# Performance work log

Measured on AMD Instinct MI355X. Metric: run time of the kernel, lower is better.

Reference implementation:

```python
import jax, jax.numpy as jnp
import numpy as np

T, B, D = 4096, 8, 256  # tgt_len, batch, embed dim
P, O = 256, 256         # proj_dim, out_dim


def setup_inputs() -> dict:
    key = jax.random.key(0)
    k1, k2, k3, k4, k5 = jax.random.split(key, 5)
    return {
        "query": jax.random.normal(k1, (T, B, D), dtype=jnp.float32),
        "W_kqv": jax.random.normal(k2, (D, 3 * P), dtype=jnp.float32) * (D ** -0.5),
        "b_kqv": jax.random.normal(k3, (3 * P,), dtype=jnp.float32) * 0.02,
        "W_out": jax.random.normal(k4, (P, O), dtype=jnp.float32) * (P ** -0.5),
        "b_out": jax.random.normal(k5, (O,), dtype=jnp.float32) * 0.02,
    }


def reference(query, W_kqv, b_kqv, W_out, b_out):
    # query: [T, B, D] (Time x Batch x Channel)
    p = W_kqv.shape[1] // 3
    scaling = p ** -0.5
    qkv = query @ W_kqv + b_kqv                      # [T, B, 3P]
    q, k, v = jnp.split(qkv, 3, axis=-1)             # each [T, B, P]
    q = (q * scaling).transpose(1, 0, 2)             # [B, T, P]
    k = k.transpose(1, 0, 2)                         # [B, S, P] (S == T)
    v = v.transpose(1, 0, 2)                         # [B, S, P]
    scores = jnp.einsum('btp,bsp->bts', q, k)        # [B, T, S]
    probs = jax.nn.softmax(scores.astype(jnp.float32), axis=-1).astype(q.dtype)
    attn = jnp.einsum('bts,bsp->btp', probs, v)      # [B, T, P]
    attn = attn.transpose(1, 0, 2)                   # [T, B, P]
    return attn @ W_out + b_out                      # [T, B, O]
```

## Files before the change

kernel.cpp:

```cpp
#include <hip/hip_runtime.h>
#include <hip/hip_bf16.h>

#define T_LEN 4096
#define BATCH 8
#define D_DIM 256
#define P_DIM 256
#define O_DIM 256
#define N3    768

typedef __bf16 bf16;
typedef __attribute__((ext_vector_type(8))) __bf16 bf16x8;
typedef __attribute__((ext_vector_type(4))) __bf16 bf16x4;
typedef __attribute__((ext_vector_type(4))) float f32x4;
typedef __attribute__((ext_vector_type(16))) float f32x16;

#define MFMA16(a, b, c) __builtin_amdgcn_mfma_f32_16x16x32_bf16(a, b, c, 0, 0, 0)
#define MFMA32(a, b, c) __builtin_amdgcn_mfma_f32_32x32x16_bf16(a, b, c, 0, 0, 0)

#define LDS_P 72

#define BARRIER_LGKM() __asm__ __volatile__("s_waitcnt lgkmcnt(0)\n\ts_barrier" ::: "memory")
#define BARRIER_VM(N) __asm__ __volatile__("s_waitcnt vmcnt(" #N ")\n\ts_barrier" ::: "memory")

typedef __attribute__((address_space(1))) const unsigned int g_u32;
typedef __attribute__((address_space(3))) unsigned int l_u32;
#define GLD16(gp, lp) __builtin_amdgcn_global_load_lds((g_u32*)(gp), (l_u32*)(lp), 16, 0, 0)

__device__ __forceinline__ void wpack_body(
    const float* __restrict__ src, bf16* __restrict__ dst, int ncols, int g)
{
    const int lane = g & 63;
    const int idx = g >> 6;
    const int nt = idx & 3, kt = (idx >> 2) & 7, ch = idx >> 5;
    const int n = ch * 64 + nt * 16 + (lane & 15);
    const int kb = kt * 32 + (lane >> 4) * 8;
    bf16x8 pk;
    #pragma unroll
    for (int j = 0; j < 8; ++j) pk[j] = (bf16)src[(size_t)(kb + j) * ncols + n];
    *(bf16x8*)&dst[(size_t)g * 8] = pk;
}

__global__ __launch_bounds__(256) void wpack_all_kernel(
    const float* __restrict__ W_kqv, const float* __restrict__ W_out,
    bf16* __restrict__ wkp, bf16* __restrict__ wop)
{
    const int bid = blockIdx.x;
    if (bid < 96) {
        wpack_body(W_kqv, wkp, N3, bid * 256 + threadIdx.x);
    } else {
        wpack_body(W_out, wop, O_DIM, (bid - 96) * 256 + threadIdx.x);
    }
}

__global__ __launch_bounds__(256) void qkv_proj_kernel(
    const float* __restrict__ query, const bf16* __restrict__ wkp,
    const float* __restrict__ b_kqv,
    bf16* __restrict__ qb, bf16* __restrict__ kpk, bf16* __restrict__ vpk)
{
    __shared__ __align__(16) bf16 Tt[64][72];
    __shared__ __align__(16) bf16 Wb[2][16384];
    const int m0 = blockIdx.x * 64;
    const int t0g = m0 >> 3;
    const int tid = threadIdx.x;
    const int lane = tid & 63, wave = tid >> 6, l15 = lane & 15, quad = lane >> 4;
    const int arow = wave * 16 + l15;

#define STAGE_W(CH, NB)                                                       \
    {                                                                         \
        const bf16* gsrc = wkp + (size_t)(CH) * 16384;                        \
        _Pragma("unroll")                                                     \
        for (int j = 0; j < 8; ++j)                                           \
            GLD16(gsrc + ((size_t)j * 256 + tid) * 8,                         \
                  &Wb[NB][(j * 256 + wave * 64) * 8]);                        \
    }

    STAGE_W(0, 0);

    bf16x8 af[8];
    {
        const float* qsrc = query + (size_t)(m0 + arow) * D_DIM + quad * 8;
        #pragma unroll
        for (int kt = 0; kt < 8; ++kt) {
            float4 f0 = *(const float4*)(qsrc + kt * 32);
            float4 f1 = *(const float4*)(qsrc + kt * 32 + 4);
            af[kt] = bf16x8{(bf16)f0.x, (bf16)f0.y, (bf16)f0.z, (bf16)f0.w,
                            (bf16)f1.x, (bf16)f1.y, (bf16)f1.z, (bf16)f1.w};
        }
    }

    for (int ch = 0; ch < 12; ++ch) {
        const int buf = ch & 1;
        if (ch < 11) {
            STAGE_W(ch + 1, buf ^ 1);
            BARRIER_VM(8);
        } else {
            BARRIER_VM(0);
        }

        f32x4 acc[4];
        #pragma unroll
        for (int i = 0; i < 4; ++i)
            for (int r = 0; r < 4; ++r) acc[i][r] = 0.f;
        #pragma unroll
        for (int kt = 0; kt < 8; ++kt) {
            #pragma unroll
            for (int nt = 0; nt < 4; ++nt) {
                bf16x8 bb = *(const bf16x8*)&Wb[buf][((kt * 4 + nt) * 64 + lane) * 8];
                acc[nt] = MFMA16(af[kt], bb, acc[nt]);
            }
        }

        BARRIER_LGKM();

        if (ch < 8) {
            const float scale = (ch < 4) ? 0.0625f : 1.0f;
            #pragma unroll
            for (int nt = 0; nt < 4; ++nt) {
                const int c = ch * 64 + nt * 16 + l15;
                const float bias = b_kqv[c];
                #pragma unroll
                for (int r = 0; r < 4; ++r)
                    Tt[wave * 16 + quad * 4 + r][nt * 16 + l15]
                        = (bf16)((acc[nt][r] + bias) * scale);
            }
            BARRIER_LGKM();
            if (ch < 4) {
                #pragma unroll
                for (int uu = 0; uu < 2; ++uu) {
                    const int u = tid * 2 + uu;
                    const int row = u >> 3, cl = u & 7;
                    bf16x8 pk = *(const bf16x8*)&Tt[row][cl * 8];
                    const int m = m0 + row, t = m >> 3, bi = m & 7;
                    *(bf16x8*)&qb[((size_t)bi * T_LEN + t) * P_DIM + ch * 64 + cl * 8] = pk;
                }
            } else {
                #pragma unroll
                for (int uu = 0; uu < 2; ++uu) {
                    const int u = tid * 2 + uu;
                    const int cl = u >> 6, bi = (u >> 3) & 7, idx = u & 7;
                    const int row = idx * 8 + bi;
                    bf16x8 pk = *(const bf16x8*)&Tt[row][cl * 8];
                    const int t = t0g + idx;
                    const int st32 = t >> 5, n31 = t & 31;
                    const int c16 = (ch - 4) * 4 + (cl >> 1), halfk = cl & 1;
                    *(bf16x8*)&kpk[(size_t)((((bi * 128 + st32) * 16 + c16) * 64
                                             + halfk * 32 + n31) * 8)] = pk;
                }
            }
        } else {
            #pragma unroll
            for (int nt = 0; nt < 4; ++nt) {
                const int c = ch * 64 + nt * 16 + l15;
                const float bias = b_kqv[c];
                #pragma unroll
                for (int r = 0; r < 4; ++r)
                    Tt[nt * 16 + l15][wave * 16 + quad * 4 + r] = (bf16)(acc[nt][r] + bias);
            }
            BARRIER_LGKM();
            const int s64 = t0g >> 6, ks = (t0g >> 4) & 3, halfv = (t0g >> 3) & 1;
            #pragma unroll
            for (int uu = 0; uu < 2; ++uu) {
                const int u = tid * 2 + uu;
                const int cl = u >> 3, bi = u & 7;
                bf16x8 pk;
                #pragma unroll
                for (int j = 0; j < 8; ++j) pk[j] = Tt[cl][j * 8 + bi];
                const int cc = (ch - 8) * 64 + cl;
                const int ptG = cc >> 5, n31 = cc & 31;
                *(bf16x8*)&vpk[((((size_t)bi * 64 + s64) * 4 + ks) * 8 + ptG) * 512
                               + (size_t)(halfv * 32 + n31) * 8] = pk;
            }
        }
    }
#undef STAGE_W
}

__global__ __launch_bounds__(256, 2) void flash_attn_kernel(
    const bf16* __restrict__ qb, const bf16* __restrict__ kpk,
    const bf16* __restrict__ vpk, const bf16* __restrict__ wop,
    const float* __restrict__ b_out, float* __restrict__ out)
{
    __shared__ __align__(16) bf16 Ps[2][64][LDS_P];
    __shared__ float l_red[2][64];
    __shared__ __align__(16) bf16 At[64][264];

    const int bid = blockIdx.x;
    const int b = bid & 7;
    const int t0 = (bid >> 3) * 64;
    const int tid = threadIdx.x;
    const int lane = tid & 63, wave = tid >> 6;
    const int l31 = lane & 31, half = lane >> 5;
    const int rg = wave & 1, sh = wave >> 1;

    bf16x8 qf[16];
    {
        const bf16* qrow = qb + ((size_t)b * T_LEN + t0 + rg * 32 + l31) * P_DIM + half * 8;
        #pragma unroll
        for (int kt = 0; kt < 16; ++kt) qf[kt] = *(const bf16x8*)(qrow + kt * 16);
    }

    f32x16 acc_o[2][2];
    float l_part[16];
    #pragma unroll
    for (int i = 0; i < 16; ++i) {
        acc_o[0][0][i] = 0.f; acc_o[0][1][i] = 0.f;
        acc_o[1][0][i] = 0.f; acc_o[1][1][i] = 0.f;
        l_part[i] = 0.f;
    }

    const bf16* kfb = kpk + (size_t)b * 128 * 16 * 512;
    const bf16* vfb = vpk + (size_t)b * 64 * 4 * 8 * 512;

    bf16x8 kpre[8];
    {
        const bf16* kf0 = kfb + ((size_t)sh * 16 * 64 + lane) * 8;
        #pragma unroll
        for (int c = 0; c < 8; ++c) kpre[c] = *(const bf16x8*)(kf0 + (size_t)c * 512);
    }

    for (int s0 = 0; s0 < T_LEN; s0 += 64) {
        const int buf = (s0 >> 6) & 1;
        const bf16* kf  = kfb + (((size_t)((s0 >> 5) + sh)) * 16 * 64 + lane) * 8;
        const bf16* kfn = kfb + (((size_t)(((s0 + 64) >> 5) + sh)) * 16 * 64 + lane) * 8;

        bf16x8 kc2[8];
        #pragma unroll
        for (int c = 0; c < 8; ++c) kc2[c] = *(const bf16x8*)(kf + (size_t)(8 + c) * 512);

        f32x16 accs;
        #pragma unroll
        for (int i = 0; i < 16; ++i) accs[i] = 0.f;
        #pragma unroll
        for (int c = 0; c < 8; ++c) accs = MFMA32(qf[c], kpre[c], accs);
        #pragma unroll
        for (int c = 0; c < 8; ++c) accs = MFMA32(qf[8 + c], kc2[c], accs);

        const bf16* vf = vfb + (((size_t)(s0 >> 6) * 4) * 8 + wave * 2) * 512 + (size_t)lane * 8;
        bf16x8 bv[8];
        #pragma unroll
        for (int ks = 0; ks < 4; ++ks) {
            bv[ks * 2]     = *(const bf16x8*)(vf + (size_t)ks * 8 * 512);
            bv[ks * 2 + 1] = *(const bf16x8*)(vf + (size_t)(ks * 8 + 1) * 512);
        }
        #pragma unroll
        for (int c = 0; c < 8; ++c) kpre[c] = *(const bf16x8*)(kfn + (size_t)c * 512);

        #pragma unroll
        for (int r = 0; r < 16; ++r) {
            float p = __expf(accs[r]);
            bf16 pb = (bf16)p;
            l_part[r] += (float)pb;
            int row = rg * 32 + (r & 3) + 8 * (r >> 2) + 4 * half;
            Ps[buf][row][sh * 32 + l31] = pb;
        }

        BARRIER_LGKM();

        #pragma unroll
        for (int ks = 0; ks < 4; ++ks) {
            bf16x8 ap0 = *(const bf16x8*)&Ps[buf][l31][ks * 16 + half * 8];
            bf16x8 ap1 = *(const bf16x8*)&Ps[buf][32 + l31][ks * 16 + half * 8];
            acc_o[0][0] = MFMA32(ap0, bv[ks * 2],     acc_o[0][0]);
            acc_o[0][1] = MFMA32(ap0, bv[ks * 2 + 1], acc_o[0][1]);
            acc_o[1][0] = MFMA32(ap1, bv[ks * 2],     acc_o[1][0]);
            acc_o[1][1] = MFMA32(ap1, bv[ks * 2 + 1], acc_o[1][1]);
        }
    }

    #pragma unroll
    for (int r = 0; r < 16; ++r) {
        float v = l_part[r];
        v += __shfl_xor(v, 1, 64);
        v += __shfl_xor(v, 2, 64);
        v += __shfl_xor(v, 4, 64);
        v += __shfl_xor(v, 8, 64);
        v += __shfl_xor(v, 16, 64);
        l_part[r] = v;
    }
    if (l31 == 0) {
        #pragma unroll
        for (int r = 0; r < 16; ++r) {
            const int row = rg * 32 + (r & 3) + 8 * (r >> 2) + 4 * half;
            l_red[sh][row] = l_part[r];
        }
    }
    __syncthreads();

    #pragma unroll
    for (int rt = 0; rt < 2; ++rt) {
        #pragma unroll
        for (int r = 0; r < 16; ++r) {
            const int row = rt * 32 + (r & 3) + 8 * (r >> 2) + 4 * half;
            const float linv = 1.0f / (l_red[0][row] + l_red[1][row]);
            At[row][wave * 64 + l31]      = (bf16)(acc_o[rt][0][r] * linv);
            At[row][wave * 64 + 32 + l31] = (bf16)(acc_o[rt][1][r] * linv);
        }
    }
    __syncthreads();

    {
        const int l15 = lane & 15, quad = lane >> 4;
        const int arow = wave * 16 + l15;
        bf16x8 af[8];
        #pragma unroll
        for (int kt = 0; kt < 8; ++kt)
            af[kt] = *(const bf16x8*)&At[arow][quad * 8 + kt * 32];

        for (int ch = 0; ch < 4; ++ch) {
            f32x4 acc[4];
            #pragma unroll
            for (int i = 0; i < 4; ++i)
                for (int r = 0; r < 4; ++r) acc[i][r] = 0.f;
            #pragma unroll
            for (int kt = 0; kt < 8; ++kt) {
                #pragma unroll
                for (int nt = 0; nt < 4; ++nt) {
                    bf16x8 bb = *(const bf16x8*)&wop[((((size_t)ch * 8 + kt) * 4 + nt) * 64 + lane) * 8];
                    acc[nt] = MFMA16(af[kt], bb, acc[nt]);
                }
            }
            #pragma unroll
            for (int nt = 0; nt < 4; ++nt) {
                const int n = ch * 64 + nt * 16 + l15;
                const float bias = b_out[n];
                #pragma unroll
                for (int r = 0; r < 4; ++r) {
                    const int t = t0 + wave * 16 + quad * 4 + r;
                    out[((size_t)t * BATCH + b) * O_DIM + n] = acc[nt][r] + bias;
                }
            }
        }
    }
}

extern "C" void kernel_launch(void* const* d_in, const int* in_sizes, int n_in,
                              void* d_out, int out_size, void* d_ws, size_t ws_size,
                              hipStream_t stream) {
    const float* query = (const float*)d_in[0];
    const float* W_kqv = (const float*)d_in[1];
    const float* b_kqv = (const float*)d_in[2];
    const float* W_out = (const float*)d_in[3];
    const float* b_out = (const float*)d_in[4];
    float* out = (float*)d_out;

    const size_t BUF = (size_t)BATCH * T_LEN * P_DIM;
    bf16* qb   = (bf16*)d_ws;
    bf16* kpk  = qb + BUF;
    bf16* vpk  = kpk + BUF;
    bf16* scr  = vpk + BUF;
    bf16* wkp  = scr;
    bf16* wop  = scr + 262144;

    wpack_all_kernel<<<128, 256, 0, stream>>>(W_kqv, W_out, wkp, wop);
    qkv_proj_kernel<<<512, 256, 0, stream>>>(query, wkp, b_kqv, qb, kpk, vpk);
    flash_attn_kernel<<<512, 256, 0, stream>>>(qb, kpk, vpk, wop, b_out, out);
}
```

Baseline: 267.9 us.

## Split QKV projection over column groups and read weights directly from global

The QKV projection kernel now launches four times as many blocks. Each block handles three of the twelve 64-column weight chunks instead of all twelve. The double-buffered LDS staging of packed weights via global_load_lds is removed, and each wave reads B fragments straight from global memory, where they should be served from L2. This aims to raise parallelism and occupancy, since the 32 KB LDS weight buffer is gone. The trade-off is that the query rows are loaded and converted four times, and the weight reads go through global memory with no LDS reuse.

```diff
diff --git a/kernel.cpp b/kernel.cpp
--- a/kernel.cpp
+++ b/kernel.cpp
@@ -20,11 +20,6 @@
 #define LDS_P 72
 
 #define BARRIER_LGKM() __asm__ __volatile__("s_waitcnt lgkmcnt(0)\n\ts_barrier" ::: "memory")
-#define BARRIER_VM(N) __asm__ __volatile__("s_waitcnt vmcnt(" #N ")\n\ts_barrier" ::: "memory")
-
-typedef __attribute__((address_space(1))) const unsigned int g_u32;
-typedef __attribute__((address_space(3))) unsigned int l_u32;
-#define GLD16(gp, lp) __builtin_amdgcn_global_load_lds((g_u32*)(gp), (l_u32*)(lp), 16, 0, 0)
 
 __device__ __forceinline__ void wpack_body(
     const float* __restrict__ src, bf16* __restrict__ dst, int ncols, int g)
@@ -58,23 +53,13 @@
     bf16* __restrict__ qb, bf16* __restrict__ kpk, bf16* __restrict__ vpk)
 {
     __shared__ __align__(16) bf16 Tt[64][72];
-    __shared__ __align__(16) bf16 Wb[2][16384];
-    const int m0 = blockIdx.x * 64;
+    const int bid = blockIdx.x;
+    const int cg = bid >> 9;
+    const int m0 = (bid & 511) * 64;
     const int t0g = m0 >> 3;
     const int tid = threadIdx.x;
     const int lane = tid & 63, wave = tid >> 6, l15 = lane & 15, quad = lane >> 4;
     const int arow = wave * 16 + l15;
-
-#define STAGE_W(CH, NB)                                                       \
-    {                                                                         \
-        const bf16* gsrc = wkp + (size_t)(CH) * 16384;                        \
-        _Pragma("unroll")                                                     \
-        for (int j = 0; j < 8; ++j)                                           \
-            GLD16(gsrc + ((size_t)j * 256 + tid) * 8,                         \
-                  &Wb[NB][(j * 256 + wave * 64) * 8]);                        \
-    }
-
-    STAGE_W(0, 0);
 
     bf16x8 af[8];
     {
@@ -88,24 +73,19 @@
         }
     }
 
-    for (int ch = 0; ch < 12; ++ch) {
-        const int buf = ch & 1;
-        if (ch < 11) {
-            STAGE_W(ch + 1, buf ^ 1);
-            BARRIER_VM(8);
-        } else {
-            BARRIER_VM(0);
-        }
+    #pragma unroll
+    for (int i = 0; i < 3; ++i) {
+        const int ch = cg * 3 + i;
 
         f32x4 acc[4];
         #pragma unroll
-        for (int i = 0; i < 4; ++i)
-            for (int r = 0; r < 4; ++r) acc[i][r] = 0.f;
+        for (int n = 0; n < 4; ++n)
+            for (int r = 0; r < 4; ++r) acc[n][r] = 0.f;
         #pragma unroll
         for (int kt = 0; kt < 8; ++kt) {
             #pragma unroll
             for (int nt = 0; nt < 4; ++nt) {
-                bf16x8 bb = *(const bf16x8*)&Wb[buf][((kt * 4 + nt) * 64 + lane) * 8];
+                bf16x8 bb = *(const bf16x8*)&wkp[((((size_t)ch * 8 + kt) * 4 + nt) * 64 + lane) * 8];
                 acc[nt] = MFMA16(af[kt], bb, acc[nt]);
             }
         }
@@ -172,7 +152,6 @@
             }
         }
     }
-#undef STAGE_W
 }
 
 __global__ __launch_bounds__(256, 2) void flash_attn_kernel(
@@ -352,6 +331,6 @@
     bf16* wop  = scr + 262144;
 
     wpack_all_kernel<<<128, 256, 0, stream>>>(W_kqv, W_out, wkp, wop);
-    qkv_proj_kernel<<<512, 256, 0, stream>>>(query, wkp, b_kqv, qb, kpk, vpk);
+    qkv_proj_kernel<<<2048, 256, 0, stream>>>(query, wkp, b_kqv, qb, kpk, vpk);
     flash_attn_kernel<<<512, 256, 0, stream>>>(qb, kpk, vpk, wop, b_out, out);
 }
```

New measurement: 280.6 us. 4.7% more time.
